# Kernel optimization log

Measured on AMD Instinct MI355X. Metric: run time of the kernel, lower is better.

Reference implementation:

```python
import jax, jax.numpy as jnp
import numpy as np

B, T, D, H, L, V = 2, 1024, 768, 12, 6, 32000
HD = D // H
EPS = 1e-5


def _ln(x, w, b):
    mu = jnp.mean(x, axis=-1, keepdims=True)
    var = jnp.mean((x - mu) ** 2, axis=-1, keepdims=True)
    return (x - mu) * jax.lax.rsqrt(var + EPS) * w + b


def setup_inputs() -> dict:
    key = jax.random.key(0)
    ks = jax.random.split(key, 20)
    s = 0.02
    inp = {
        "idx": jax.random.randint(ks[0], (B, T), 0, V),
        "wte": jax.random.normal(ks[1], (V, D), jnp.float32) * s,
        "wpe": jax.random.normal(ks[2], (T, D), jnp.float32) * s,
        # per-layer stacked params (leading dim L)
        "ln1_w": jnp.ones((L, D), jnp.float32),
        "ln1_b": jnp.zeros((L, D), jnp.float32),
        "attn_w": jax.random.normal(ks[3], (L, D, 3 * D), jnp.float32) * s,
        "attn_b": jnp.zeros((L, 3 * D), jnp.float32),
        "proj_w": jax.random.normal(ks[4], (L, D, D), jnp.float32) * s,
        "proj_b": jnp.zeros((L, D), jnp.float32),
        "ln2_w": jnp.ones((L, D), jnp.float32),
        "ln2_b": jnp.zeros((L, D), jnp.float32),
        "fc_w": jax.random.normal(ks[5], (L, D, 4 * D), jnp.float32) * s,
        "fc_b": jnp.zeros((L, 4 * D), jnp.float32),
        "fcproj_w": jax.random.normal(ks[6], (L, 4 * D, D), jnp.float32) * s,
        "fcproj_b": jnp.zeros((L, D), jnp.float32),
        "lnf_w": jnp.ones((D,), jnp.float32),
        "lnf_b": jnp.zeros((D,), jnp.float32),
        "head_w": jax.random.normal(ks[7], (D, V), jnp.float32) * s,
    }
    return inp


def _forward(idx, wte, wpe, ln1_w, ln1_b, attn_w, attn_b, proj_w, proj_b,
             ln2_w, ln2_b, fc_w, fc_b, fcproj_w, fcproj_b, lnf_w, lnf_b, head_w):
    t = idx.shape[1]
    x = wte[idx] + wpe[:t][None]  # [B,T,D]
    causal = jnp.tril(jnp.ones((t, t), bool))
    neg_inf = jnp.asarray(-jnp.inf, x.dtype)
    scale = 1.0 / np.sqrt(HD)

    def block(x, p):
        l1w, l1b, aw, ab, pw, pb, l2w, l2b, fw, fb, fpw, fpb = p
        h = _ln(x, l1w, l1b)
        qkv = h @ aw + ab  # [B,T,3D]
        q, k, v = jnp.split(qkv, 3, axis=-1)
        q = q.reshape(B, t, H, HD).transpose(0, 2, 1, 3)
        k = k.reshape(B, t, H, HD).transpose(0, 2, 1, 3)
        v = v.reshape(B, t, H, HD).transpose(0, 2, 1, 3)
        att = jnp.einsum('bhqd,bhkd->bhqk', q, k) * scale
        att = jnp.where(causal, att, neg_inf)
        att = jax.nn.softmax(att, axis=-1)
        y = jnp.einsum('bhqk,bhkd->bhqd', att, v)
        y = y.transpose(0, 2, 1, 3).reshape(B, t, D) @ pw + pb
        x = x + y
        h2 = _ln(x, l2w, l2b)
        m = jax.nn.gelu(h2 @ fw + fb, approximate=False) @ fpw + fpb
        return x + m, None

    layer_params = (ln1_w, ln1_b, attn_w, attn_b, proj_w, proj_b,
                    ln2_w, ln2_b, fc_w, fc_b, fcproj_w, fcproj_b)
    x, _ = jax.lax.scan(block, x, layer_params)
    logits = _ln(x, lnf_w, lnf_b) @ head_w  # [B,T,V]
    return logits


def reference(idx, wte, wpe, ln1_w, ln1_b, attn_w, attn_b, proj_w, proj_b,
              ln2_w, ln2_b, fc_w, fc_b, fcproj_w, fcproj_b, lnf_w, lnf_b, head_w):
    return _forward(idx, wte, wpe, ln1_w, ln1_b, attn_w, attn_b, proj_w, proj_b,
                    ln2_w, ln2_b, fc_w, fc_b, fcproj_w, fcproj_b, lnf_w, lnf_b, head_w)
```

## Files before the change

kernel.cpp:

```cpp
#include <hip/hip_runtime.h>
#include <hip/hip_bf16.h>
#include <math.h>

static constexpr int Bv = 2, Tv = 1024, Dv = 768, Hv = 12, Lv = 6, Vv = 32000, HDv = 64;
static constexpr int MROWS = Bv * Tv;

typedef __attribute__((ext_vector_type(8))) short bf16x8;
typedef __attribute__((ext_vector_type(8))) short short8;
typedef __attribute__((ext_vector_type(4))) short short4v;
typedef __attribute__((ext_vector_type(4))) float f32x4;

typedef __attribute__((address_space(1))) const void gvoid;
typedef __attribute__((address_space(3))) void svoid;
__device__ __forceinline__ void gld16(const void* g, void* s) {
  __builtin_amdgcn_global_load_lds((gvoid*)g, (svoid*)s, 16, 0, 0);
}
__device__ __forceinline__ short f2bf(float v) {
  __hip_bfloat16 hb = __float2bfloat16(v);
  return *reinterpret_cast<short*>(&hb);
}
__device__ __forceinline__ int xcd_remap(int lin, int nwg) {
  int q = nwg >> 3, r = nwg & 7;
  int xcd = lin & 7, idx = lin >> 3;
  return (xcd < r ? xcd * (q + 1) : r * (q + 1) + (xcd - r) * q) + idx;
}

__global__ __launch_bounds__(256) void embed_kernel(const int* __restrict__ idx,
                                                    const float* __restrict__ wte,
                                                    const float* __restrict__ wpe,
                                                    float* __restrict__ x) {
  int i4 = blockIdx.x * 256 + threadIdx.x;
  int total = MROWS * Dv / 4;
  if (i4 >= total) return;
  int d4 = (i4 % (Dv / 4)) * 4;
  int bt = i4 / (Dv / 4);
  int t  = bt % Tv;
  int id = idx[bt];
  float4 a = *(const float4*)(wte + (size_t)id * Dv + d4);
  float4 p = *(const float4*)(wpe + (size_t)t  * Dv + d4);
  a.x += p.x; a.y += p.y; a.z += p.z; a.w += p.w;
  *(float4*)(x + (size_t)bt * Dv + d4) = a;
}

__device__ __forceinline__ void ln_body(const float* __restrict__ x,
                                        const float* __restrict__ w,
                                        const float* __restrict__ b,
                                        __hip_bfloat16* __restrict__ out, int row) {
  __shared__ float red[8];
  const float* xr = x + (size_t)row * Dv;
  int tid = threadIdx.x;
  float v0 = xr[tid], v1 = xr[tid + 256], v2 = xr[tid + 512];
  int wid = tid >> 6, lane = tid & 63;

  float s = v0 + v1 + v2;
  #pragma unroll
  for (int off = 1; off < 64; off <<= 1) s += __shfl_xor(s, off, 64);
  if (lane == 0) red[wid] = s;
  __syncthreads();
  s = red[0] + red[1] + red[2] + red[3];
  float mu = s * (1.0f / Dv);

  float d0 = v0 - mu, d1 = v1 - mu, d2 = v2 - mu;
  float q = d0 * d0 + d1 * d1 + d2 * d2;
  #pragma unroll
  for (int off = 1; off < 64; off <<= 1) q += __shfl_xor(q, off, 64);
  if (lane == 0) red[4 + wid] = q;
  __syncthreads();
  q = red[4] + red[5] + red[6] + red[7];
  float rs = rsqrtf(q * (1.0f / Dv) + 1e-5f);

  __hip_bfloat16* orow = out + (size_t)row * Dv;
  orow[tid]       = __float2bfloat16(d0 * rs * w[tid]       + b[tid]);
  orow[tid + 256] = __float2bfloat16(d1 * rs * w[tid + 256] + b[tid + 256]);
  orow[tid + 512] = __float2bfloat16(d2 * rs * w[tid + 512] + b[tid + 512]);
}

__global__ __launch_bounds__(256) void ln_kernel(const float* __restrict__ x,
                                                 const float* __restrict__ w,
                                                 const float* __restrict__ b,
                                                 __hip_bfloat16* __restrict__ out) {
  ln_body(x, w, b, out, blockIdx.x);
}

__device__ __forceinline__ void tcast_body(const float* __restrict__ W,
                                           __hip_bfloat16* __restrict__ Wt,
                                           int K, int N, int k0, int n0) {
  __shared__ float tile[32][33];
  int tx = threadIdx.x & 31, ty = threadIdx.x >> 5;
  #pragma unroll
  for (int r = 0; r < 32; r += 8)
    tile[ty + r][tx] = W[(size_t)(k0 + ty + r) * N + n0 + tx];
  __syncthreads();
  #pragma unroll
  for (int r = 0; r < 32; r += 8)
    Wt[(size_t)(n0 + ty + r) * K + k0 + tx] = __float2bfloat16(tile[tx][ty + r]);
}

__global__ __launch_bounds__(256) void ln_tcast4_kernel(const float* __restrict__ x,
                                                        const float* __restrict__ lw,
                                                        const float* __restrict__ lb,
                                                        __hip_bfloat16* __restrict__ h,
                                                        const float* __restrict__ s0,
                                                        const float* __restrict__ s1,
                                                        const float* __restrict__ s2,
                                                        const float* __restrict__ s3,
                                                        __hip_bfloat16* __restrict__ d0,
                                                        __hip_bfloat16* __restrict__ d1,
                                                        __hip_bfloat16* __restrict__ d2,
                                                        __hip_bfloat16* __restrict__ d3) {
  int blk = blockIdx.x;
  if (blk < MROWS) { ln_body(x, lw, lb, h, blk); return; }
  int lin = blk - MROWS;
  const float* W; __hip_bfloat16* Wt; int K, N, loc;
  if (lin < 1728)      { W = s0; Wt = d0; K = 768;  N = 2304; loc = lin; }
  else if (lin < 2304) { W = s1; Wt = d1; K = 768;  N = 768;  loc = lin - 1728; }
  else if (lin < 4608) { W = s2; Wt = d2; K = 768;  N = 3072; loc = lin - 2304; }
  else                 { W = s3; Wt = d3; K = 3072; N = 768;  loc = lin - 4608; }
  int nb = N / 32;
  tcast_body(W, Wt, K, N, (loc / nb) * 32, (loc % nb) * 32);
}

__global__ __launch_bounds__(256) void lnf_tcast_kernel(const float* __restrict__ x,
                                                        const float* __restrict__ lw,
                                                        const float* __restrict__ lb,
                                                        __hip_bfloat16* __restrict__ h,
                                                        const float* __restrict__ head_w,
                                                        __hip_bfloat16* __restrict__ wb) {
  int blk = blockIdx.x;
  if (blk < MROWS) { ln_body(x, lw, lb, h, blk); return; }
  int loc = blk - MROWS;
  int nb = Vv / 32;
  tcast_body(head_w, wb, Dv, Vv, (loc / nb) * 32, (loc % nb) * 32);
}

template <bool GELU, bool OBF, bool VT>
__device__ __forceinline__ void gemm128_body(const __hip_bfloat16* __restrict__ A,
                                             const __hip_bfloat16* __restrict__ Wt,
                                             const float* __restrict__ bias,
                                             const float* __restrict__ resid,
                                             void* __restrict__ outv,
                                             __hip_bfloat16* __restrict__ vt,
                                             int M, int N, int K) {
  __shared__ short As[2][8192];
  __shared__ short Bs[2][8192];
  int nwg = gridDim.x * gridDim.y;
  int wgid = xcd_remap(blockIdx.y * gridDim.x + blockIdx.x, nwg);
  int m0 = (wgid % gridDim.x) * 128, n0 = (wgid / gridDim.x) * 128;

  int tid = threadIdx.x;
  int w = tid >> 6, lane = tid & 63;
  int wr = w >> 1, wc = w & 1;
  int lr = lane & 15, lk = lane >> 4;

  f32x4 acc[4][4];
  #pragma unroll
  for (int m = 0; m < 4; ++m)
    #pragma unroll
    for (int n = 0; n < 4; ++n) acc[m][n] = (f32x4){0.f, 0.f, 0.f, 0.f};

  auto stg = [&](int k0, int p) {
    #pragma unroll
    for (int e = 0; e < 4; ++e) {
      int idx2 = e * 256 + tid;
      int r = idx2 >> 3, g = idx2 & 7;
      int gs = (g ^ (r & 7)) * 8;
      gld16(A  + (size_t)(m0 + r) * K + k0 + gs, &As[p][idx2 * 8]);
      gld16(Wt + (size_t)(n0 + r) * K + k0 + gs, &Bs[p][idx2 * 8]);
    }
  };

  stg(0, 0);
  __syncthreads();
  int NK = K >> 6;
  for (int kt = 0; kt < NK; ++kt) {
    int p = kt & 1;
    if (kt + 1 < NK) stg((kt + 1) << 6, p ^ 1);
    bf16x8 af[4][2], bf[4][2];
    #pragma unroll
    for (int m = 0; m < 4; ++m) {
      int ra = wr * 64 + m * 16 + lr;
      #pragma unroll
      for (int kf = 0; kf < 2; ++kf)
        af[m][kf] = *(const bf16x8*)(&As[p][ra * 64 + (((kf * 4 + lk) ^ (ra & 7)) * 8)]);
    }
    #pragma unroll
    for (int n = 0; n < 4; ++n) {
      int rb = wc * 64 + n * 16 + lr;
      #pragma unroll
      for (int kf = 0; kf < 2; ++kf)
        bf[n][kf] = *(const bf16x8*)(&Bs[p][rb * 64 + (((kf * 4 + lk) ^ (rb & 7)) * 8)]);
    }
    #pragma unroll
    for (int kf = 0; kf < 2; ++kf)
      #pragma unroll
      for (int m = 0; m < 4; ++m)
        #pragma unroll
        for (int n = 0; n < 4; ++n)
          acc[m][n] = __builtin_amdgcn_mfma_f32_16x16x32_bf16(af[m][kf], bf[n][kf], acc[m][n], 0, 0, 0);
    __syncthreads();
  }

  int row0 = m0 + wr * 64, col0 = n0 + wc * 64;
  float* outf = (float*)outv;
  __hip_bfloat16* outb = (__hip_bfloat16*)outv;
  #pragma unroll
  for (int n = 0; n < 4; ++n) {
    int col = col0 + n * 16 + lr;
    float bv = bias ? bias[col] : 0.f;
    #pragma unroll
    for (int m = 0; m < 4; ++m) {
      int rbase = row0 + m * 16 + lk * 4;
      float r4[4];
      #pragma unroll
      for (int j = 0; j < 4; ++j) {
        float v = acc[m][n][j] + bv;
        if (GELU) v = 0.5f * v * (1.0f + erff(v * 0.70710678118f));
        size_t o = (size_t)(rbase + j) * N + col;
        if (resid) v += resid[o];
        r4[j] = v;
        if (OBF) outb[o] = __float2bfloat16(v);
        else     outf[o] = v;
      }
      if (VT && col >= 2 * Dv) {
        int hh = (col - 2 * Dv) >> 6, dd = (col - 2 * Dv) & 63;
        int bb = rbase >> 10, t0 = rbase & 1023;
        short4v pk = {f2bf(r4[0]), f2bf(r4[1]), f2bf(r4[2]), f2bf(r4[3])};
        *(short4v*)(vt + (((size_t)(bb * Hv + hh) * HDv + dd) << 10) + t0) = pk;
      }
    }
  }
}

__global__ __launch_bounds__(256) void qkv_gemm_kernel(const __hip_bfloat16* A,
                                                       const __hip_bfloat16* Wt,
                                                       const float* bias,
                                                       void* outv, __hip_bfloat16* vt,
                                                       int M, int N, int K) {
  gemm128_body<false, true, true>(A, Wt, bias, nullptr, outv, vt, M, N, K);
}
__global__ __launch_bounds__(256) void fc_gemm_kernel(const __hip_bfloat16* A,
                                                      const __hip_bfloat16* Wt,
                                                      const float* bias,
                                                      void* outv, int M, int N, int K) {
  gemm128_body<true, true, false>(A, Wt, bias, nullptr, outv, nullptr, M, N, K);
}

__device__ __forceinline__ void gemm64_body(const __hip_bfloat16* __restrict__ A,
                                            const __hip_bfloat16* __restrict__ Wt,
                                            const float* __restrict__ bias,
                                            const float* __restrict__ resid,
                                            float* __restrict__ out,
                                            int M, int N, int K) {
  __shared__ short As[2][4096];
  __shared__ short Bs[2][4096];
  int nwg = gridDim.x * gridDim.y;
  int wgid = xcd_remap(blockIdx.y * gridDim.x + blockIdx.x, nwg);
  int m0 = (wgid % gridDim.x) * 64, n0 = (wgid / gridDim.x) * 64;

  int tid = threadIdx.x;
  int w = tid >> 6, lane = tid & 63;
  int wr = w >> 1, wc = w & 1;
  int lr = lane & 15, lk = lane >> 4;
  int rsub = lane >> 3, go = lane & 7;

  f32x4 acc[2][2];
  #pragma unroll
  for (int m = 0; m < 2; ++m)
    #pragma unroll
    for (int n = 0; n < 2; ++n) acc[m][n] = (f32x4){0.f, 0.f, 0.f, 0.f};

  auto stg = [&](int k0, int p) {
    #pragma unroll
    for (int e = 0; e < 2; ++e) {
      int row = w * 16 + e * 8 + rsub;
      int gs = (go ^ rsub) * 8;
      gld16(A  + (size_t)(m0 + row) * K + k0 + gs, &As[p][w * 1024 + e * 512]);
      gld16(Wt + (size_t)(n0 + row) * K + k0 + gs, &Bs[p][w * 1024 + e * 512]);
    }
  };

  stg(0, 0);
  __syncthreads();
  int NK = K >> 6;
  for (int kt = 0; kt < NK; ++kt) {
    int p = kt & 1;
    if (kt + 1 < NK) stg((kt + 1) << 6, p ^ 1);
    #pragma unroll
    for (int kf = 0; kf < 2; ++kf) {
      bf16x8 af[2], bf[2];
      #pragma unroll
      for (int m = 0; m < 2; ++m) {
        int row = wr * 32 + m * 16 + lr;
        af[m] = *(const bf16x8*)(&As[p][row * 64 + (((kf * 4 + lk) ^ (row & 7)) * 8)]);
      }
      #pragma unroll
      for (int n = 0; n < 2; ++n) {
        int row = wc * 32 + n * 16 + lr;
        bf[n] = *(const bf16x8*)(&Bs[p][row * 64 + (((kf * 4 + lk) ^ (row & 7)) * 8)]);
      }
      #pragma unroll
      for (int m = 0; m < 2; ++m)
        #pragma unroll
        for (int n = 0; n < 2; ++n)
          acc[m][n] = __builtin_amdgcn_mfma_f32_16x16x32_bf16(af[m], bf[n], acc[m][n], 0, 0, 0);
    }
    __syncthreads();
  }

  int row0 = m0 + wr * 32, col0 = n0 + wc * 32;
  #pragma unroll
  for (int n = 0; n < 2; ++n) {
    int col = col0 + n * 16 + lr;
    float bv = bias ? bias[col] : 0.f;
    #pragma unroll
    for (int m = 0; m < 2; ++m) {
      int rbase = row0 + m * 16 + lk * 4;
      #pragma unroll
      for (int j = 0; j < 4; ++j) {
        float v = acc[m][n][j] + bv;
        size_t o = (size_t)(rbase + j) * N + col;
        if (resid) v += resid[o];
        out[o] = v;
      }
    }
  }
}

__global__ __launch_bounds__(256) void proj_gemm_kernel(const __hip_bfloat16* A,
                                                        const __hip_bfloat16* Wt,
                                                        const float* bias,
                                                        const float* resid, float* out,
                                                        int M, int N, int K) {
  gemm64_body(A, Wt, bias, resid, out, M, N, K);
}
__global__ __launch_bounds__(256) void fcproj_gemm_kernel(const __hip_bfloat16* A,
                                                          const __hip_bfloat16* Wt,
                                                          const float* bias,
                                                          const float* resid, float* out,
                                                          int M, int N, int K) {
  gemm64_body(A, Wt, bias, resid, out, M, N, K);
}

__global__ __launch_bounds__(512, 2) void gemm256_kernel(const __hip_bfloat16* __restrict__ A,
                                                         const __hip_bfloat16* __restrict__ Wt,
                                                         float* __restrict__ out,
                                                         int N, int K) {
  __shared__ short lds[65536];
  int nwg = gridDim.x * gridDim.y;
  int wgid = xcd_remap(blockIdx.y * gridDim.x + blockIdx.x, nwg);
  int m0 = (wgid % gridDim.x) * 256, n0 = (wgid / gridDim.x) * 256;

  int tid = threadIdx.x;
  int w = tid >> 6, lane = tid & 63;
  int wr = w >> 2, wc = w & 3;
  int lr = lane & 15, lk = lane >> 4;

  f32x4 acc[8][4];
  #pragma unroll
  for (int m = 0; m < 8; ++m)
    #pragma unroll
    for (int n = 0; n < 4; ++n) acc[m][n] = (f32x4){0.f, 0.f, 0.f, 0.f};

  int NT = K >> 6;

  auto stage = [&](int tau, int h) {
    int tsrc = tau < NT ? tau : NT - 1;
    const __hip_bfloat16* mat;
    size_t rb; int lofs;
    if (h == 0)      { mat = A;  rb = (size_t)m0;       lofs = 0; }
    else if (h == 1) { mat = Wt; rb = (size_t)n0;       lofs = 16384; }
    else if (h == 2) { mat = Wt; rb = (size_t)n0 + 128; lofs = 24576; }
    else             { mat = A;  rb = (size_t)m0 + 128; lofs = 8192; }
    short* lb = lds + (tau & 1) * 32768 + lofs;
    #pragma unroll
    for (int e = 0; e < 2; ++e) {
      int idx = e * 512 + tid;
      int r = idx >> 3, g = idx & 7;
      gld16(mat + (rb + r) * (size_t)K + tsrc * 64 + ((g ^ (r & 7)) * 8), lb + idx * 8);
    }
  };

  stage(0, 0); stage(0, 1); stage(0, 2); stage(0, 3);
  asm volatile("s_waitcnt vmcnt(4)" ::: "memory");
  asm volatile("s_barrier" ::: "memory");

  for (int tau = 0; tau < NT; ++tau) {
    const short* bufA = lds + (tau & 1) * 32768;
    const short* bufB = bufA + 16384;
    #pragma unroll
    for (int q = 0; q < 4; ++q) {
      stage(tau + 1, q);
      asm volatile("s_waitcnt vmcnt(4)" ::: "memory");
      int qm = q >> 1, qn = q & 1;
      const short* ab = bufA + qm * 8192;
      const short* bb = bufB + qn * 8192;
      bf16x8 af[4][2], bf[2][2];
      #pragma unroll
      for (int mi = 0; mi < 4; ++mi) {
        int ra = wr * 64 + mi * 16 + lr;
        #pragma unroll
        for (int kf = 0; kf < 2; ++kf)
          af[mi][kf] = *(const bf16x8*)(ab + ra * 64 + (((kf * 4 + lk) ^ (ra & 7)) * 8));
      }
      #pragma unroll
      for (int ni = 0; ni < 2; ++ni) {
        int rb2 = wc * 32 + ni * 16 + lr;
        #pragma unroll
        for (int kf = 0; kf < 2; ++kf)
          bf[ni][kf] = *(const bf16x8*)(bb + rb2 * 64 + (((kf * 4 + lk) ^ (rb2 & 7)) * 8));
      }
      asm volatile("s_barrier" ::: "memory");
      __builtin_amdgcn_s_setprio(1);
      #pragma unroll
      for (int mi = 0; mi < 4; ++mi)
        #pragma unroll
        for (int ni = 0; ni < 2; ++ni)
          #pragma unroll
          for (int kf = 0; kf < 2; ++kf)
            acc[qm * 4 + mi][qn * 2 + ni] = __builtin_amdgcn_mfma_f32_16x16x32_bf16(
                af[mi][kf], bf[ni][kf], acc[qm * 4 + mi][qn * 2 + ni], 0, 0, 0);
      __builtin_amdgcn_s_setprio(0);
      asm volatile("s_barrier" ::: "memory");
    }
  }

  #pragma unroll
  for (int gm = 0; gm < 8; ++gm) {
    int row = m0 + (gm >> 2) * 128 + wr * 64 + (gm & 3) * 16 + lk * 4;
    #pragma unroll
    for (int gn = 0; gn < 4; ++gn) {
      int col = n0 + (gn >> 1) * 128 + wc * 32 + (gn & 1) * 16 + lr;
      #pragma unroll
      for (int j = 0; j < 4; ++j)
        out[(size_t)(row + j) * N + col] = acc[gm][gn][j];
    }
  }
}

__global__ __launch_bounds__(256) void attn_kernel(const __hip_bfloat16* __restrict__ qkv,
                                                   const __hip_bfloat16* __restrict__ vt,
                                                   __hip_bfloat16* __restrict__ y) {
  __shared__ short Ks[2][4096];
  __shared__ short Vts[2][4096];
  __shared__ short Ps[4][1024];
  int b = blockIdx.z, h = blockIdx.y;
  int qb = (gridDim.x - 1 - blockIdx.x) * 64;
  int tid = threadIdx.x;
  int w = tid >> 6, l = tid & 63;
  int lr = l & 15, lk = l >> 4;

  bf16x8 aq[2];
  {
    const __hip_bfloat16* qp = qkv + ((size_t)(b * Tv + qb + w * 16 + lr)) * 3 * Dv + h * HDv + lk * 8;
    aq[0] = *(const bf16x8*)qp;
    aq[1] = *(const bf16x8*)(qp + 32);
  }

  f32x4 o[4];
  #pragma unroll
  for (int n = 0; n < 4; ++n) o[n] = (f32x4){0.f, 0.f, 0.f, 0.f};
  float mrow[4] = {-1e30f, -1e30f, -1e30f, -1e30f};
  float lrow[4] = {0.f, 0.f, 0.f, 0.f};

  int r8 = l >> 3, c8 = l & 7;
  int nt = qb / 64 + 1;

  auto stageKV = [&](int kt2, int p) {
    int kbase = kt2 * 64;
    #pragma unroll
    for (int e = 0; e < 2; ++e) {
      int r0 = w * 16 + e * 8;
      int rK = r0 + r8;
      int csK = c8 ^ (rK & 7);
      gld16(qkv + ((size_t)(b * Tv + kbase + rK)) * 3 * Dv + Dv + h * HDv + csK * 8,
            &Ks[p][r0 * 64]);
      gld16(vt + ((size_t)((b * Hv + h) * HDv + rK)) * Tv + kbase + csK * 8,
            &Vts[p][r0 * 64]);
    }
  };

  stageKV(0, 0);
  __syncthreads();

  for (int kt = 0; kt < nt; ++kt) {
    int p = kt & 1;
    if (kt + 1 < nt) stageKV(kt + 1, p ^ 1);

    f32x4 s[4];
    #pragma unroll
    for (int n = 0; n < 4; ++n) s[n] = (f32x4){0.f, 0.f, 0.f, 0.f};
    __builtin_amdgcn_s_setprio(1);
    #pragma unroll
    for (int kf = 0; kf < 2; ++kf)
      #pragma unroll
      for (int nf = 0; nf < 4; ++nf) {
        int row = nf * 16 + lr;
        int g = (kf * 4 + lk) ^ (row & 7);
        bf16x8 bk = *(const bf16x8*)(&Ks[p][row * 64 + g * 8]);
        s[nf] = __builtin_amdgcn_mfma_f32_16x16x32_bf16(aq[kf], bk, s[nf], 0, 0, 0);
      }
    __builtin_amdgcn_s_setprio(0);
    #pragma unroll
    for (int nf = 0; nf < 4; ++nf)
      #pragma unroll
      for (int j = 0; j < 4; ++j) s[nf][j] *= 0.125f;

    if (kt == nt - 1) {
      #pragma unroll
      for (int nf = 0; nf < 4; ++nf) {
        int kl = nf * 16 + lr;
        #pragma unroll
        for (int j = 0; j < 4; ++j)
          if (kl > w * 16 + lk * 4 + j) s[nf][j] = -1e30f;
      }
    }

    float sc[4];
    #pragma unroll
    for (int j = 0; j < 4; ++j) {
      float pm = fmaxf(fmaxf(s[0][j], s[1][j]), fmaxf(s[2][j], s[3][j]));
      pm = fmaxf(pm, __shfl_xor(pm, 1, 64));
      pm = fmaxf(pm, __shfl_xor(pm, 2, 64));
      pm = fmaxf(pm, __shfl_xor(pm, 4, 64));
      pm = fmaxf(pm, __shfl_xor(pm, 8, 64));
      float mn = fmaxf(mrow[j], pm);
      sc[j] = __expf(mrow[j] - mn);
      mrow[j] = mn;
    }
    #pragma unroll
    for (int j = 0; j < 4; ++j) {
      float ls = 0.f;
      #pragma unroll
      for (int nf = 0; nf < 4; ++nf) {
        float p2 = __expf(s[nf][j] - mrow[j]);
        s[nf][j] = p2;
        ls += p2;
      }
      ls += __shfl_xor(ls, 1, 64);
      ls += __shfl_xor(ls, 2, 64);
      ls += __shfl_xor(ls, 4, 64);
      ls += __shfl_xor(ls, 8, 64);
      lrow[j] = lrow[j] * sc[j] + ls;
    }
    #pragma unroll
    for (int n = 0; n < 4; ++n)
      #pragma unroll
      for (int j = 0; j < 4; ++j) o[n][j] *= sc[j];

    short* pw = Ps[w];
    #pragma unroll
    for (int nf = 0; nf < 4; ++nf)
      #pragma unroll
      for (int j = 0; j < 4; ++j) {
        int ql = lk * 4 + j, k = nf * 16 + lr;
        pw[ql * 64 + (((k >> 3) ^ (ql & 7)) * 8) + (k & 7)] = f2bf(s[nf][j]);
      }
    bf16x8 pa[2];
    #pragma unroll
    for (int kf = 0; kf < 2; ++kf) {
      int g = (kf * 4 + lk) ^ (lr & 7);
      pa[kf] = *(const bf16x8*)(pw + lr * 64 + g * 8);
    }
    __builtin_amdgcn_s_setprio(1);
    #pragma unroll
    for (int kf = 0; kf < 2; ++kf)
      #pragma unroll
      for (int nf = 0; nf < 4; ++nf) {
        int d = nf * 16 + lr;
        int g = (kf * 4 + lk) ^ (d & 7);
        bf16x8 bv = *(const bf16x8*)(&Vts[p][d * 64 + g * 8]);
        o[nf] = __builtin_amdgcn_mfma_f32_16x16x32_bf16(pa[kf], bv, o[nf], 0, 0, 0);
      }
    __builtin_amdgcn_s_setprio(0);
    __syncthreads();
  }

  #pragma unroll
  for (int j = 0; j < 4; ++j) lrow[j] = 1.f / lrow[j];
  #pragma unroll
  for (int nf = 0; nf < 4; ++nf)
    #pragma unroll
    for (int j = 0; j < 4; ++j) {
      size_t oidx = ((size_t)(b * Tv + qb + w * 16 + lk * 4 + j)) * Dv + h * HDv + nf * 16 + lr;
      y[oidx] = __float2bfloat16(o[nf][j] * lrow[j]);
    }
}

extern "C" void kernel_launch(void* const* d_in, const int* in_sizes, int n_in,
                              void* d_out, int out_size, void* d_ws, size_t ws_size,
                              hipStream_t stream) {
  const int*   idx      = (const int*)  d_in[0];
  const float* wte      = (const float*)d_in[1];
  const float* wpe      = (const float*)d_in[2];
  const float* ln1_w    = (const float*)d_in[3];
  const float* ln1_b    = (const float*)d_in[4];
  const float* attn_w   = (const float*)d_in[5];
  const float* attn_b   = (const float*)d_in[6];
  const float* proj_w   = (const float*)d_in[7];
  const float* proj_b   = (const float*)d_in[8];
  const float* ln2_w    = (const float*)d_in[9];
  const float* ln2_b    = (const float*)d_in[10];
  const float* fc_w     = (const float*)d_in[11];
  const float* fc_b     = (const float*)d_in[12];
  const float* fcproj_w = (const float*)d_in[13];
  const float* fcproj_b = (const float*)d_in[14];
  const float* lnf_w    = (const float*)d_in[15];
  const float* lnf_b    = (const float*)d_in[16];
  const float* head_w   = (const float*)d_in[17];
  float* outp = (float*)d_out;

  char* w8 = (char*)d_ws;
  float*          x    = (float*)w8;
  __hip_bfloat16* h    = (__hip_bfloat16*)(w8 + 6291456);
  __hip_bfloat16* qkv  = (__hip_bfloat16*)(w8 + 9437184);
  __hip_bfloat16* m4   = qkv;
  __hip_bfloat16* y    = (__hip_bfloat16*)(w8 + 22020096);
  __hip_bfloat16* vt   = (__hip_bfloat16*)(w8 + 25165824);
  __hip_bfloat16* wbuf = (__hip_bfloat16*)(w8 + 28311552);

  __hip_bfloat16* wb_attn   = wbuf;
  __hip_bfloat16* wb_proj   = wb_attn + (size_t)768 * 2304;
  __hip_bfloat16* wb_fc     = wb_proj + (size_t)768 * 768;
  __hip_bfloat16* wb_fcproj = wb_fc   + (size_t)768 * 3072;

  embed_kernel<<<(MROWS * Dv / 4 + 255) / 256, 256, 0, stream>>>(idx, wte, wpe, x);

  for (int l = 0; l < Lv; ++l) {
    ln_tcast4_kernel<<<MROWS + 6912, 256, 0, stream>>>(
        x, ln1_w + (size_t)l * Dv, ln1_b + (size_t)l * Dv, h,
        attn_w   + (size_t)l * Dv * 3 * Dv,
        proj_w   + (size_t)l * Dv * Dv,
        fc_w     + (size_t)l * Dv * 4 * Dv,
        fcproj_w + (size_t)l * 4 * Dv * Dv,
        wb_attn, wb_proj, wb_fc, wb_fcproj);
    qkv_gemm_kernel<<<dim3(MROWS / 128, 3 * Dv / 128), 256, 0, stream>>>(
        h, wb_attn, attn_b + (size_t)l * 3 * Dv, qkv, vt, MROWS, 3 * Dv, Dv);
    attn_kernel<<<dim3(Tv / 64, Hv, Bv), 256, 0, stream>>>(qkv, vt, y);
    proj_gemm_kernel<<<dim3(MROWS / 64, Dv / 64), 256, 0, stream>>>(
        y, wb_proj, proj_b + (size_t)l * Dv, x, x, MROWS, Dv, Dv);
    ln_kernel<<<MROWS, 256, 0, stream>>>(x, ln2_w + (size_t)l * Dv, ln2_b + (size_t)l * Dv, h);
    fc_gemm_kernel<<<dim3(MROWS / 128, 4 * Dv / 128), 256, 0, stream>>>(
        h, wb_fc, fc_b + (size_t)l * 4 * Dv, m4, MROWS, 4 * Dv, Dv);
    fcproj_gemm_kernel<<<dim3(MROWS / 64, Dv / 64), 256, 0, stream>>>(
        m4, wb_fcproj, fcproj_b + (size_t)l * Dv, x, x, MROWS, Dv, 4 * Dv);
  }

  lnf_tcast_kernel<<<MROWS + 24000, 256, 0, stream>>>(
      x, lnf_w, lnf_b, h, head_w, wbuf);
  gemm256_kernel<<<dim3(MROWS / 256, Vv / 256), 512, 0, stream>>>(
      h, wbuf, outp, Vv, Dv);
}
```

Baseline: 1.058 ms.

## Shrink QKV and FC GEMM tiles and flatten attention grid ordering

The QKV GEMM moves from 128x128 to 64x64 tiles. The FC GEMM becomes a dedicated 128x64 kernel with fused GELU. The attention kernel uses a 1D grid that interleaves batch and head so the longest causal query blocks are scheduled first across all heads. The aim is more workgroups per GEMM to fill the many compute units, and better load balance in attention. The cost is less operand reuse per tile and more global and LDS traffic.

```diff
diff --git a/kernel.cpp b/kernel.cpp
--- a/kernel.cpp
+++ b/kernel.cpp
@@ -134,38 +134,38 @@
 }
 
 template <bool GELU, bool OBF, bool VT>
-__device__ __forceinline__ void gemm128_body(const __hip_bfloat16* __restrict__ A,
-                                             const __hip_bfloat16* __restrict__ Wt,
-                                             const float* __restrict__ bias,
-                                             const float* __restrict__ resid,
-                                             void* __restrict__ outv,
-                                             __hip_bfloat16* __restrict__ vt,
-                                             int M, int N, int K) {
-  __shared__ short As[2][8192];
-  __shared__ short Bs[2][8192];
+__device__ __forceinline__ void gemm64_body(const __hip_bfloat16* __restrict__ A,
+                                            const __hip_bfloat16* __restrict__ Wt,
+                                            const float* __restrict__ bias,
+                                            const float* __restrict__ resid,
+                                            void* __restrict__ outv,
+                                            __hip_bfloat16* __restrict__ vt,
+                                            int M, int N, int K) {
+  __shared__ short As[2][4096];
+  __shared__ short Bs[2][4096];
   int nwg = gridDim.x * gridDim.y;
   int wgid = xcd_remap(blockIdx.y * gridDim.x + blockIdx.x, nwg);
-  int m0 = (wgid % gridDim.x) * 128, n0 = (wgid / gridDim.x) * 128;
+  int m0 = (wgid % gridDim.x) * 64, n0 = (wgid / gridDim.x) * 64;
 
   int tid = threadIdx.x;
   int w = tid >> 6, lane = tid & 63;
   int wr = w >> 1, wc = w & 1;
   int lr = lane & 15, lk = lane >> 4;
-
-  f32x4 acc[4][4];
-  #pragma unroll
-  for (int m = 0; m < 4; ++m)
-    #pragma unroll
-    for (int n = 0; n < 4; ++n) acc[m][n] = (f32x4){0.f, 0.f, 0.f, 0.f};
+  int rsub = lane >> 3, go = lane & 7;
+
+  f32x4 acc[2][2];
+  #pragma unroll
+  for (int m = 0; m < 2; ++m)
+    #pragma unroll
+    for (int n = 0; n < 2; ++n) acc[m][n] = (f32x4){0.f, 0.f, 0.f, 0.f};
 
   auto stg = [&](int k0, int p) {
     #pragma unroll
-    for (int e = 0; e < 4; ++e) {
-      int idx2 = e * 256 + tid;
-      int r = idx2 >> 3, g = idx2 & 7;
-      int gs = (g ^ (r & 7)) * 8;
-      gld16(A  + (size_t)(m0 + r) * K + k0 + gs, &As[p][idx2 * 8]);
-      gld16(Wt + (size_t)(n0 + r) * K + k0 + gs, &Bs[p][idx2 * 8]);
+    for (int e = 0; e < 2; ++e) {
+      int row = w * 16 + e * 8 + rsub;
+      int gs = (go ^ rsub) * 8;
+      gld16(A  + (size_t)(m0 + row) * K + k0 + gs, &As[p][w * 1024 + e * 512]);
+      gld16(Wt + (size_t)(n0 + row) * K + k0 + gs, &Bs[p][w * 1024 + e * 512]);
     }
   };
 
@@ -175,40 +175,37 @@
   for (int kt = 0; kt < NK; ++kt) {
     int p = kt & 1;
     if (kt + 1 < NK) stg((kt + 1) << 6, p ^ 1);
-    bf16x8 af[4][2], bf[4][2];
-    #pragma unroll
-    for (int m = 0; m < 4; ++m) {
-      int ra = wr * 64 + m * 16 + lr;
-      #pragma unroll
-      for (int kf = 0; kf < 2; ++kf)
-        af[m][kf] = *(const bf16x8*)(&As[p][ra * 64 + (((kf * 4 + lk) ^ (ra & 7)) * 8)]);
-    }
-    #pragma unroll
-    for (int n = 0; n < 4; ++n) {
-      int rb = wc * 64 + n * 16 + lr;
-      #pragma unroll
-      for (int kf = 0; kf < 2; ++kf)
-        bf[n][kf] = *(const bf16x8*)(&Bs[p][rb * 64 + (((kf * 4 + lk) ^ (rb & 7)) * 8)]);
-    }
-    #pragma unroll
-    for (int kf = 0; kf < 2; ++kf)
-      #pragma unroll
-      for (int m = 0; m < 4; ++m)
+    #pragma unroll
+    for (int kf = 0; kf < 2; ++kf) {
+      bf16x8 af[2], bf[2];
+      #pragma unroll
+      for (int m = 0; m < 2; ++m) {
+        int row = wr * 32 + m * 16 + lr;
+        af[m] = *(const bf16x8*)(&As[p][row * 64 + (((kf * 4 + lk) ^ (row & 7)) * 8)]);
+      }
+      #pragma unroll
+      for (int n = 0; n < 2; ++n) {
+        int row = wc * 32 + n * 16 + lr;
+        bf[n] = *(const bf16x8*)(&Bs[p][row * 64 + (((kf * 4 + lk) ^ (row & 7)) * 8)]);
+      }
+      #pragma unroll
+      for (int m = 0; m < 2; ++m)
         #pragma unroll
-        for (int n = 0; n < 4; ++n)
-          acc[m][n] = __builtin_amdgcn_mfma_f32_16x16x32_bf16(af[m][kf], bf[n][kf], acc[m][n], 0, 0, 0);
+        for (int n = 0; n < 2; ++n)
+          acc[m][n] = __builtin_amdgcn_mfma_f32_16x16x32_bf16(af[m], bf[n], acc[m][n], 0, 0, 0);
+    }
     __syncthreads();
   }
 
-  int row0 = m0 + wr * 64, col0 = n0 + wc * 64;
+  int row0 = m0 + wr * 32, col0 = n0 + wc * 32;
   float* outf = (float*)outv;
   __hip_bfloat16* outb = (__hip_bfloat16*)outv;
   #pragma unroll
-  for (int n = 0; n < 4; ++n) {
+  for (int n = 0; n < 2; ++n) {
     int col = col0 + n * 16 + lr;
     float bv = bias ? bias[col] : 0.f;
     #pragma unroll
-    for (int m = 0; m < 4; ++m) {
+    for (int m = 0; m < 2; ++m) {
       int rbase = row0 + m * 16 + lk * 4;
       float r4[4];
       #pragma unroll
@@ -236,46 +233,59 @@
                                                        const float* bias,
                                                        void* outv, __hip_bfloat16* vt,
                                                        int M, int N, int K) {
-  gemm128_body<false, true, true>(A, Wt, bias, nullptr, outv, vt, M, N, K);
-}
-__global__ __launch_bounds__(256) void fc_gemm_kernel(const __hip_bfloat16* A,
-                                                      const __hip_bfloat16* Wt,
-                                                      const float* bias,
-                                                      void* outv, int M, int N, int K) {
-  gemm128_body<true, true, false>(A, Wt, bias, nullptr, outv, nullptr, M, N, K);
-}
-
-__device__ __forceinline__ void gemm64_body(const __hip_bfloat16* __restrict__ A,
-                                            const __hip_bfloat16* __restrict__ Wt,
-                                            const float* __restrict__ bias,
-                                            const float* __restrict__ resid,
-                                            float* __restrict__ out,
-                                            int M, int N, int K) {
-  __shared__ short As[2][4096];
+  gemm64_body<false, true, true>(A, Wt, bias, nullptr, outv, vt, M, N, K);
+}
+__global__ __launch_bounds__(256) void proj_gemm_kernel(const __hip_bfloat16* A,
+                                                        const __hip_bfloat16* Wt,
+                                                        const float* bias,
+                                                        const float* resid, float* out,
+                                                        int M, int N, int K) {
+  gemm64_body<false, false, false>(A, Wt, bias, resid, out, nullptr, M, N, K);
+}
+__global__ __launch_bounds__(256) void fcproj_gemm_kernel(const __hip_bfloat16* A,
+                                                          const __hip_bfloat16* Wt,
+                                                          const float* bias,
+                                                          const float* resid, float* out,
+                                                          int M, int N, int K) {
+  gemm64_body<false, false, false>(A, Wt, bias, resid, out, nullptr, M, N, K);
+}
+
+__global__ __launch_bounds__(256) void fc_gemm_kernel(const __hip_bfloat16* __restrict__ A,
+                                                      const __hip_bfloat16* __restrict__ Wt,
+                                                      const float* __restrict__ bias,
+                                                      void* __restrict__ outv,
+                                                      int M, int N, int K) {
+  __shared__ short As[2][8192];
   __shared__ short Bs[2][4096];
   int nwg = gridDim.x * gridDim.y;
   int wgid = xcd_remap(blockIdx.y * gridDim.x + blockIdx.x, nwg);
-  int m0 = (wgid % gridDim.x) * 64, n0 = (wgid / gridDim.x) * 64;
+  int m0 = (wgid % gridDim.x) * 128, n0 = (wgid / gridDim.x) * 64;
 
   int tid = threadIdx.x;
   int w = tid >> 6, lane = tid & 63;
   int wr = w >> 1, wc = w & 1;
   int lr = lane & 15, lk = lane >> 4;
-  int rsub = lane >> 3, go = lane & 7;
-
-  f32x4 acc[2][2];
-  #pragma unroll
-  for (int m = 0; m < 2; ++m)
+
+  f32x4 acc[4][2];
+  #pragma unroll
+  for (int m = 0; m < 4; ++m)
     #pragma unroll
     for (int n = 0; n < 2; ++n) acc[m][n] = (f32x4){0.f, 0.f, 0.f, 0.f};
 
   auto stg = [&](int k0, int p) {
     #pragma unroll
+    for (int e = 0; e < 4; ++e) {
+      int idx2 = e * 256 + tid;
+      int r = idx2 >> 3, g = idx2 & 7;
+      int gs = (g ^ (r & 7)) * 8;
+      gld16(A + (size_t)(m0 + r) * K + k0 + gs, &As[p][idx2 * 8]);
+    }
+    #pragma unroll
     for (int e = 0; e < 2; ++e) {
-      int row = w * 16 + e * 8 + rsub;
-      int gs = (go ^ rsub) * 8;
-      gld16(A  + (size_t)(m0 + row) * K + k0 + gs, &As[p][w * 1024 + e * 512]);
-      gld16(Wt + (size_t)(n0 + row) * K + k0 + gs, &Bs[p][w * 1024 + e * 512]);
+      int idx2 = e * 256 + tid;
+      int r = idx2 >> 3, g = idx2 & 7;
+      int gs = (g ^ (r & 7)) * 8;
+      gld16(Wt + (size_t)(n0 + r) * K + k0 + gs, &Bs[p][idx2 * 8]);
     }
   };
 
@@ -287,10 +297,10 @@
     if (kt + 1 < NK) stg((kt + 1) << 6, p ^ 1);
     #pragma unroll
     for (int kf = 0; kf < 2; ++kf) {
-      bf16x8 af[2], bf[2];
-      #pragma unroll
-      for (int m = 0; m < 2; ++m) {
-        int row = wr * 32 + m * 16 + lr;
+      bf16x8 af[4], bf[2];
+      #pragma unroll
+      for (int m = 0; m < 4; ++m) {
+        int row = wr * 64 + m * 16 + lr;
         af[m] = *(const bf16x8*)(&As[p][row * 64 + (((kf * 4 + lk) ^ (row & 7)) * 8)]);
       }
       #pragma unroll
@@ -299,7 +309,7 @@
         bf[n] = *(const bf16x8*)(&Bs[p][row * 64 + (((kf * 4 + lk) ^ (row & 7)) * 8)]);
       }
       #pragma unroll
-      for (int m = 0; m < 2; ++m)
+      for (int m = 0; m < 4; ++m)
         #pragma unroll
         for (int n = 0; n < 2; ++n)
           acc[m][n] = __builtin_amdgcn_mfma_f32_16x16x32_bf16(af[m], bf[n], acc[m][n], 0, 0, 0);
@@ -307,38 +317,23 @@
     __syncthreads();
   }
 
-  int row0 = m0 + wr * 32, col0 = n0 + wc * 32;
+  int row0 = m0 + wr * 64, col0 = n0 + wc * 32;
+  __hip_bfloat16* outb = (__hip_bfloat16*)outv;
   #pragma unroll
   for (int n = 0; n < 2; ++n) {
     int col = col0 + n * 16 + lr;
-    float bv = bias ? bias[col] : 0.f;
-    #pragma unroll
-    for (int m = 0; m < 2; ++m) {
+    float bv = bias[col];
+    #pragma unroll
+    for (int m = 0; m < 4; ++m) {
       int rbase = row0 + m * 16 + lk * 4;
       #pragma unroll
       for (int j = 0; j < 4; ++j) {
         float v = acc[m][n][j] + bv;
-        size_t o = (size_t)(rbase + j) * N + col;
-        if (resid) v += resid[o];
-        out[o] = v;
-      }
-    }
-  }
-}
-
-__global__ __launch_bounds__(256) void proj_gemm_kernel(const __hip_bfloat16* A,
-                                                        const __hip_bfloat16* Wt,
-                                                        const float* bias,
-                                                        const float* resid, float* out,
-                                                        int M, int N, int K) {
-  gemm64_body(A, Wt, bias, resid, out, M, N, K);
-}
-__global__ __launch_bounds__(256) void fcproj_gemm_kernel(const __hip_bfloat16* A,
-                                                          const __hip_bfloat16* Wt,
-                                                          const float* bias,
-                                                          const float* resid, float* out,
-                                                          int M, int N, int K) {
-  gemm64_body(A, Wt, bias, resid, out, M, N, K);
+        v = 0.5f * v * (1.0f + erff(v * 0.70710678118f));
+        outb[(size_t)(rbase + j) * N + col] = __float2bfloat16(v);
+      }
+    }
+  }
 }
 
 __global__ __launch_bounds__(512, 2) void gemm256_kernel(const __hip_bfloat16* __restrict__ A,
@@ -443,8 +438,10 @@
   __shared__ short Ks[2][4096];
   __shared__ short Vts[2][4096];
   __shared__ short Ps[4][1024];
-  int b = blockIdx.z, h = blockIdx.y;
-  int qb = (gridDim.x - 1 - blockIdx.x) * 64;
+  int lin = blockIdx.x;
+  int bh = lin % 24;
+  int b = bh / Hv, h = bh % Hv;
+  int qb = (Tv / 64 - 1 - lin / 24) * 64;
   int tid = threadIdx.x;
   int w = tid >> 6, l = tid & 63;
   int lr = l & 15, lk = l >> 4;
@@ -633,13 +630,13 @@
         fc_w     + (size_t)l * Dv * 4 * Dv,
         fcproj_w + (size_t)l * 4 * Dv * Dv,
         wb_attn, wb_proj, wb_fc, wb_fcproj);
-    qkv_gemm_kernel<<<dim3(MROWS / 128, 3 * Dv / 128), 256, 0, stream>>>(
+    qkv_gemm_kernel<<<dim3(MROWS / 64, 3 * Dv / 64), 256, 0, stream>>>(
         h, wb_attn, attn_b + (size_t)l * 3 * Dv, qkv, vt, MROWS, 3 * Dv, Dv);
-    attn_kernel<<<dim3(Tv / 64, Hv, Bv), 256, 0, stream>>>(qkv, vt, y);
+    attn_kernel<<<(Tv / 64) * Hv * Bv, 256, 0, stream>>>(qkv, vt, y);
     proj_gemm_kernel<<<dim3(MROWS / 64, Dv / 64), 256, 0, stream>>>(
         y, wb_proj, proj_b + (size_t)l * Dv, x, x, MROWS, Dv, Dv);
     ln_kernel<<<MROWS, 256, 0, stream>>>(x, ln2_w + (size_t)l * Dv, ln2_b + (size_t)l * Dv, h);
-    fc_gemm_kernel<<<dim3(MROWS / 128, 4 * Dv / 128), 256, 0, stream>>>(
+    fc_gemm_kernel<<<dim3(MROWS / 128, 4 * Dv / 64), 256, 0, stream>>>(
         h, wb_fc, fc_b + (size_t)l * 4 * Dv, m4, MROWS, 4 * Dv, Dv);
     fcproj_gemm_kernel<<<dim3(MROWS / 64, Dv / 64), 256, 0, stream>>>(
         m4, wb_fcproj, fcproj_b + (size_t)l * Dv, x, x, MROWS, Dv, 4 * Dv);
```

Measured after the change: 987.8 us. -6.6%, faster.
